# Performance work log

Hardware: AMD Instinct MI355X
Metric: run time of the kernel (lower is better)

Reference implementation:

```python
import jax, jax.numpy as jnp
import numpy as np

# Module constants (from source defaults)
KERNEL_SIZES = (2, 3, 4, 5)
KERNEL_NUMS = (2, 3, 4, 5)  # sum = 14 -> fc in_features
EMB_DIM = 100
NUM_CLASSES = 5
VOCAB = 100000
B, L = 512, 512


def setup_inputs() -> dict:
    key = jax.random.key(0)
    ks = jax.random.split(key, 12)
    words = jax.random.randint(ks[0], (B, L), 0, VOCAB)
    # Dense w2v table replacing the per-token vocab/gensim lookup (OOV rows would be zeros;
    # a random dense table is equivalent math for the gather).
    emb_table = jax.random.normal(ks[1], (VOCAB, EMB_DIM), dtype=jnp.float32) * 0.1
    inp = {"words": words, "emb_table": emb_table}
    for i, (ksz, knum) in enumerate(zip(KERNEL_SIZES, KERNEL_NUMS)):
        inp[f"w{ksz}"] = jax.random.normal(ks[2 + i], (knum, EMB_DIM, ksz), dtype=jnp.float32) * 0.05
        inp[f"b{ksz}"] = jnp.zeros((knum,), dtype=jnp.float32)
    inp["fc_w"] = jax.random.normal(ks[10], (NUM_CLASSES, sum(KERNEL_NUMS)), dtype=jnp.float32) * 0.1
    inp["fc_b"] = jnp.zeros((NUM_CLASSES,), dtype=jnp.float32)
    return inp


def _conv_relu_maxpool(x, w, b):
    # x: [B, D, L], w: [O, D, k] -> conv1d VALID, relu, max over time -> [B, O]
    y = jax.lax.conv_general_dilated(
        x, w, window_strides=(1,), padding="VALID",
        dimension_numbers=("NCH", "OIH", "NCH"))
    y = jax.nn.relu(y + b[None, :, None])
    return jnp.max(y, axis=-1)


def reference(words, emb_table, w2, b2, w3, b3, w4, b4, w5, b5, fc_w, fc_b):
    # Embedding gather (replaces the serial per-token Python loop)
    x = emb_table[words]                 # [B, L, D]
    x = jnp.transpose(x, (0, 2, 1))      # [B, D, L]
    feats = jnp.concatenate([
        _conv_relu_maxpool(x, w2, b2),
        _conv_relu_maxpool(x, w3, b3),
        _conv_relu_maxpool(x, w4, b4),
        _conv_relu_maxpool(x, w5, b5),
    ], axis=1)                           # [B, 14]
    # dropout is identity at inference
    return feats @ fc_w.T + fc_b         # [B, NUM_CLASSES]
```

## Files before the change

kernel.cpp:

```cpp
#include <hip/hip_runtime.h>
#include <hip/hip_bf16.h>

#define BATCH 512
#define SEQL  512
#define NCH   14
#define NCLS  5
#define DPAD  128
#define KSTEPS 20
#define POSB  64
#define ROWS  68
#define BLKS_PER_ROW 8
#define NBLK  (BATCH * BLKS_PER_ROW)
#define WS_B_BYTES 20480
#define BIAS_OFF   20480
#define FEAT_OFF   20544
#define NIT   9

typedef __attribute__((ext_vector_type(8))) short bf16x8;
typedef __attribute__((ext_vector_type(4))) float f32x4;

static __device__ __forceinline__ unsigned short bf16bits(float f) {
    __hip_bfloat16 h = __float2bfloat16(f);
    return __builtin_bit_cast(unsigned short, h);
}

__global__ void repack_w(
    const float* __restrict__ w2, const float* __restrict__ b2,
    const float* __restrict__ w3, const float* __restrict__ b3,
    const float* __restrict__ w4, const float* __restrict__ b4,
    const float* __restrict__ w5, const float* __restrict__ b5,
    unsigned short* __restrict__ wsb, float* __restrict__ biasf)
{
    const float* WP[4] = {w2, w3, w4, w5};
    const int gi = blockIdx.x * 256 + threadIdx.x;
    if (gi < WS_B_BYTES / 2) {
        int kstep = gi >> 9;
        int rem   = gi & 511;
        int l     = rem >> 3;
        int e     = rem & 7;
        int k     = kstep * 32 + ((l >> 4) << 3) + e;
        int n     = l & 15;
        int j     = k >> 7;
        int d     = k & 127;
        float v = 0.f;
        if (n < NCH && d < 100) {
            int kc = 2 + (n >= 2) + (n >= 5) + (n >= 9);
            if (j < kc) {
                int grp = (n >= 2) + (n >= 5) + (n >= 9);
                int ob  = (grp == 0) ? 0 : (grp == 1) ? 2 : (grp == 2) ? 5 : 9;
                v = WP[grp][((n - ob) * 100 + d) * kc + j];
            }
        }
        wsb[gi] = bf16bits(v);
    }
    if (blockIdx.x == 0 && threadIdx.x < 16) {
        const int t = threadIdx.x;
        float bv = 0.f;
        if (t < 2)        bv = b2[t];
        else if (t < 5)   bv = b3[t - 2];
        else if (t < 9)   bv = b4[t - 5];
        else if (t < NCH) bv = b5[t - 9];
        biasf[t] = bv;
    }
}

__global__ __launch_bounds__(256, 8) void cnn_mfma(
    const int* __restrict__ words,
    const float* __restrict__ emb,
    const char* __restrict__ ws,
    float* __restrict__ feats)
{
    __shared__ unsigned short xs[ROWS * DPAD];
    __shared__ float red[4][16];

    const int bid = blockIdx.x;
    const int b   = bid >> 3;
    const int blk = bid & 7;
    const int p0  = blk * POSB;
    const int tid = threadIdx.x;
    const int l   = tid & 63;
    const int wv  = tid >> 6;

    int toks[NIT];
    #pragma unroll
    for (int it = 0; it < NIT; ++it) {
        const int i = tid + it * 256;
        const int r = i >> 5;
        const int t = p0 + r;
        toks[it] = (i < ROWS * 32 && t < SEQL) ? words[b * SEQL + t] : -1;
    }

    const float4* __restrict__ emb4 = reinterpret_cast<const float4*>(emb);
    uint2* xs2 = reinterpret_cast<uint2*>(xs);
    #pragma unroll
    for (int it = 0; it < NIT; ++it) {
        const int i = tid + it * 256;
        if (i < ROWS * 32) {
            const int r = i >> 5;
            const int q = i & 31;
            uint lo = 0, hi = 0;
            if (toks[it] >= 0 && q < 25) {
                float4 x = emb4[(long)toks[it] * 25 + q];
                lo = (uint)bf16bits(x.x) | ((uint)bf16bits(x.y) << 16);
                hi = (uint)bf16bits(x.z) | ((uint)bf16bits(x.w) << 16);
            }
            const int addr = (r * 256 + q * 8) ^ ((r & 7) << 4);
            xs2[addr >> 3] = make_uint2(lo, hi);
        }
    }
    __syncthreads();

    f32x4 acc = {0.f, 0.f, 0.f, 0.f};
    const int m0 = wv * 16 + (l & 15);
    const int dl = (l >> 4) << 3;
    const char* xsb = reinterpret_cast<const char*>(xs);
    #pragma unroll
    for (int ks = 0; ks < KSTEPS; ++ks) {
        const int j  = ks >> 2;
        const int d0 = ((ks & 3) << 5) + dl;
        const int row = m0 + j;
        const int aad = (row * 256 + d0 * 2) ^ ((row & 7) << 4);
        bf16x8 a = *reinterpret_cast<const bf16x8*>(xsb + aad);
        bf16x8 bf = *reinterpret_cast<const bf16x8*>(ws + (ks * 64 + l) * 16);
        acc = __builtin_amdgcn_mfma_f32_16x16x32_bf16(a, bf, acc, 0, 0, 0);
    }

    const int ch  = l & 15;
    const int kch = 2 + (ch >= 2) + (ch >= 5) + (ch >= 9);
    const float bias = *reinterpret_cast<const float*>(ws + BIAS_OFF + ch * 4);
    const int rbase = (l >> 4) << 2;
    float v = 0.f;
    #pragma unroll
    for (int r = 0; r < 4; ++r) {
        const int t = p0 + wv * 16 + rbase + r;
        if (t + kch <= SEQL) v = fmaxf(v, fmaxf(acc[r] + bias, 0.f));
    }
    v = fmaxf(v, __shfl_xor(v, 16, 64));
    v = fmaxf(v, __shfl_xor(v, 32, 64));
    if (l < 16) red[wv][ch] = v;
    __syncthreads();

    if (tid < 16) {
        float f = fmaxf(fmaxf(red[0][tid], red[1][tid]),
                        fmaxf(red[2][tid], red[3][tid]));
        feats[bid * 16 + tid] = f;
    }
}

__global__ void fc_kernel(const float* __restrict__ feats,
                          const float* __restrict__ fcw,
                          const float* __restrict__ fcb,
                          float* __restrict__ out)
{
    const int i = blockIdx.x * 256 + threadIdx.x;
    if (i >= BATCH * NCLS) return;
    const int b   = i / NCLS;
    const int cls = i - b * NCLS;
    const float* fb = feats + b * (16 * BLKS_PER_ROW);
    float acc = fcb[cls];
    #pragma unroll
    for (int o = 0; o < NCH; ++o) {
        float f = fb[o];
        #pragma unroll
        for (int w = 1; w < BLKS_PER_ROW; ++w) f = fmaxf(f, fb[w * 16 + o]);
        acc += fcw[cls * NCH + o] * f;
    }
    out[i] = acc;
}

extern "C" void kernel_launch(void* const* d_in, const int* in_sizes, int n_in,
                              void* d_out, int out_size, void* d_ws, size_t ws_size,
                              hipStream_t stream) {
    const int*   words = (const int*)  d_in[0];
    const float* emb   = (const float*)d_in[1];
    const float* w2    = (const float*)d_in[2];
    const float* b2    = (const float*)d_in[3];
    const float* w3    = (const float*)d_in[4];
    const float* b3    = (const float*)d_in[5];
    const float* w4    = (const float*)d_in[6];
    const float* b4    = (const float*)d_in[7];
    const float* w5    = (const float*)d_in[8];
    const float* b5    = (const float*)d_in[9];
    const float* fcw   = (const float*)d_in[10];
    const float* fcb   = (const float*)d_in[11];
    float* out = (float*)d_out;
    char*  ws  = (char*)d_ws;

    unsigned short* wsb  = (unsigned short*)ws;
    float* biasf = (float*)(ws + BIAS_OFF);
    float* feats = (float*)(ws + FEAT_OFF);

    hipLaunchKernelGGL(repack_w, dim3(40), dim3(256), 0, stream,
                       w2, b2, w3, b3, w4, b4, w5, b5, wsb, biasf);
    hipLaunchKernelGGL(cnn_mfma, dim3(NBLK), dim3(256), 0, stream,
                       words, emb, ws, feats);
    hipLaunchKernelGGL(fc_kernel, dim3((BATCH * NCLS + 255) / 256), dim3(256), 0, stream,
                       feats, fcw, fcb, out);
}
```

Before: 39.71 us.

## Precompute per-vocab conv tap contributions then gather, max-pool and FC per batch

Instead of gathering embeddings per token and running the conv GEMM per position, a GEMM over the whole vocabulary table computes each word's contribution to every (tap, channel) pair and stores it as bf16. A second kernel gathers five contribution rows per position, sums the taps, applies bias, ReLU and max-pool, and folds in the FC layer, which removes the separate fc kernel. This trades work proportional to B*L*D for work proportional to VOCAB*D (a 40MB table read) and adds a 12.8MB intermediate write plus an extra bf16 rounding of the partial sums.

```diff
diff --git a/kernel.cpp b/kernel.cpp
--- a/kernel.cpp
+++ b/kernel.cpp
@@ -3,18 +3,14 @@
 
 #define BATCH 512
 #define SEQL  512
+#define VOCAB 100000
 #define NCH   14
 #define NCLS  5
-#define DPAD  128
-#define KSTEPS 20
-#define POSB  64
-#define ROWS  68
-#define BLKS_PER_ROW 8
-#define NBLK  (BATCH * BLKS_PER_ROW)
-#define WS_B_BYTES 20480
-#define BIAS_OFF   20480
-#define FEAT_OFF   20544
-#define NIT   9
+
+
+#define WSB_OFF     0
+#define BIAS_OFF    16384
+#define CONTRIB_OFF 32768
 
 typedef __attribute__((ext_vector_type(8))) short bf16x8;
 typedef __attribute__((ext_vector_type(4))) float f32x4;
@@ -22,6 +18,12 @@
 static __device__ __forceinline__ unsigned short bf16bits(float f) {
     __hip_bfloat16 h = __float2bfloat16(f);
     return __builtin_bit_cast(unsigned short, h);
+}
+static __device__ __forceinline__ float bf16f(unsigned int hbits) {
+    union { unsigned int u; float f; } x; x.u = hbits << 16; return x.f;
+}
+static __device__ __forceinline__ unsigned int getdw(const uint4& u, int w) {
+    switch (w) { case 0: return u.x; case 1: return u.y; case 2: return u.z; default: return u.w; }
 }
 
 __global__ void repack_w(
@@ -33,23 +35,25 @@
 {
     const float* WP[4] = {w2, w3, w4, w5};
     const int gi = blockIdx.x * 256 + threadIdx.x;
-    if (gi < WS_B_BYTES / 2) {
-        int kstep = gi >> 9;
-        int rem   = gi & 511;
-        int l     = rem >> 3;
-        int e     = rem & 7;
-        int k     = kstep * 32 + ((l >> 4) << 3) + e;
-        int n     = l & 15;
-        int j     = k >> 7;
-        int d     = k & 127;
+    if (gi < 8192) {
+        int nt = gi >> 11;
+        int ks = (gi >> 9) & 3;
+        int l  = (gi >> 3) & 63;
+        int e  = gi & 7;
+        int n  = nt * 16 + (l & 15);
+        int k  = ks * 32 + ((l >> 4) << 3) + e;
+        int j = -1, c = 0;
+        if (n < 14)                 { j = 0; c = n; }
+        else if (n >= 16 && n < 30) { j = 1; c = n - 16; }
+        else if (n >= 32 && n < 44) { j = 2; c = 2 + (n - 32); }
+        else if (n >= 44 && n < 53) { j = 3; c = 5 + (n - 44); }
+        else if (n >= 53 && n < 58) { j = 4; c = 9 + (n - 53); }
         float v = 0.f;
-        if (n < NCH && d < 100) {
-            int kc = 2 + (n >= 2) + (n >= 5) + (n >= 9);
-            if (j < kc) {
-                int grp = (n >= 2) + (n >= 5) + (n >= 9);
-                int ob  = (grp == 0) ? 0 : (grp == 1) ? 2 : (grp == 2) ? 5 : 9;
-                v = WP[grp][((n - ob) * 100 + d) * kc + j];
-            }
+        if (j >= 0 && k < 100) {
+            int kc  = 2 + (c >= 2) + (c >= 5) + (c >= 9);
+            int grp = (c >= 2) + (c >= 5) + (c >= 9);
+            int ob  = (grp == 0) ? 0 : (grp == 1) ? 2 : (grp == 2) ? 5 : 9;
+            v = WP[grp][((c - ob) * 100 + k) * kc + j];
         }
         wsb[gi] = bf16bits(v);
     }
@@ -64,108 +68,141 @@
     }
 }
 
-__global__ __launch_bounds__(256, 8) void cnn_mfma(
-    const int* __restrict__ words,
+__global__ __launch_bounds__(256, 4) void contrib_gemm(
     const float* __restrict__ emb,
     const char* __restrict__ ws,
-    float* __restrict__ feats)
+    unsigned short* __restrict__ contrib)
 {
-    __shared__ unsigned short xs[ROWS * DPAD];
-    __shared__ float red[4][16];
-
-    const int bid = blockIdx.x;
-    const int b   = bid >> 3;
-    const int blk = bid & 7;
-    const int p0  = blk * POSB;
+    __shared__ unsigned short xs[64 * 128];
+    const int v0  = blockIdx.x * 64;
     const int tid = threadIdx.x;
     const int l   = tid & 63;
-    const int wv  = tid >> 6;
-
-    int toks[NIT];
-    #pragma unroll
-    for (int it = 0; it < NIT; ++it) {
+    const int wt  = tid >> 6;
+
+    const float4* __restrict__ emb4 = reinterpret_cast<const float4*>(emb);
+    uint2* xs2 = reinterpret_cast<uint2*>(xs);
+    #pragma unroll
+    for (int it = 0; it < 8; ++it) {
         const int i = tid + it * 256;
         const int r = i >> 5;
-        const int t = p0 + r;
-        toks[it] = (i < ROWS * 32 && t < SEQL) ? words[b * SEQL + t] : -1;
-    }
-
-    const float4* __restrict__ emb4 = reinterpret_cast<const float4*>(emb);
-    uint2* xs2 = reinterpret_cast<uint2*>(xs);
-    #pragma unroll
-    for (int it = 0; it < NIT; ++it) {
-        const int i = tid + it * 256;
-        if (i < ROWS * 32) {
-            const int r = i >> 5;
-            const int q = i & 31;
-            uint lo = 0, hi = 0;
-            if (toks[it] >= 0 && q < 25) {
-                float4 x = emb4[(long)toks[it] * 25 + q];
-                lo = (uint)bf16bits(x.x) | ((uint)bf16bits(x.y) << 16);
-                hi = (uint)bf16bits(x.z) | ((uint)bf16bits(x.w) << 16);
+        const int q = i & 31;
+        const int v = v0 + r;
+        uint lo = 0, hi = 0;
+        if (v < VOCAB && q < 25) {
+            float4 x = emb4[(long)v * 25 + q];
+            lo = (uint)bf16bits(x.x) | ((uint)bf16bits(x.y) << 16);
+            hi = (uint)bf16bits(x.z) | ((uint)bf16bits(x.w) << 16);
+        }
+        const int addr = (r * 256 + q * 8) ^ ((r & 7) << 4);
+        xs2[addr >> 3] = make_uint2(lo, hi);
+    }
+    __syncthreads();
+
+    f32x4 acc[4] = {{0.f,0.f,0.f,0.f},{0.f,0.f,0.f,0.f},
+                    {0.f,0.f,0.f,0.f},{0.f,0.f,0.f,0.f}};
+    const char* xsb = reinterpret_cast<const char*>(xs);
+    const int arow = wt * 16 + (l & 15);
+    const int dl   = (l >> 4) << 3;
+    #pragma unroll
+    for (int ks = 0; ks < 4; ++ks) {
+        const int aad = (arow * 256 + (ks * 32 + dl) * 2) ^ ((arow & 7) << 4);
+        bf16x8 a = *reinterpret_cast<const bf16x8*>(xsb + aad);
+        #pragma unroll
+        for (int nt = 0; nt < 4; ++nt) {
+            bf16x8 bf = *reinterpret_cast<const bf16x8*>(
+                ws + WSB_OFF + ((nt * 4 + ks) * 64 + l) * 16);
+            acc[nt] = __builtin_amdgcn_mfma_f32_16x16x32_bf16(a, bf, acc[nt], 0, 0, 0);
+        }
+    }
+
+    const int vbase = v0 + wt * 16 + ((l >> 4) << 2);
+    #pragma unroll
+    for (int nt = 0; nt < 4; ++nt) {
+        #pragma unroll
+        for (int r = 0; r < 4; ++r) {
+            const int v = vbase + r;
+            if (v < VOCAB)
+                contrib[(long)v * 64 + nt * 16 + (l & 15)] = bf16bits(acc[nt][r]);
+        }
+    }
+}
+
+__global__ __launch_bounds__(512, 4) void gather_max_fc(
+    const int* __restrict__ words,
+    const unsigned short* __restrict__ contrib,
+    const float* __restrict__ biasf,
+    const float* __restrict__ fcw, const float* __restrict__ fcb,
+    float* __restrict__ out)
+{
+    __shared__ float red[8][NCH];
+    __shared__ float sfin[NCH];
+
+    const int b  = blockIdx.x;
+    const int t  = threadIdx.x;
+    const int l  = t & 63;
+    const int wv = t >> 6;
+
+    constexpr int KC[NCH]  = {2,2, 3,3,3, 4,4,4,4, 5,5,5,5,5};
+    constexpr int SIDX[5]  = {0,16,32,44,53};
+    constexpr int CST[5]   = {0,0,2,5,9};
+    constexpr int B0[5]    = {0,2,4,5,6};
+
+    int tok[5];
+    #pragma unroll
+    for (int j = 0; j < 5; ++j) {
+        int u = t + j; if (u > SEQL - 1) u = SEQL - 1;
+        tok[j] = words[b * SEQL + u];
+    }
+
+    uint4 u0[5], u1[5];
+    #pragma unroll
+    for (int j = 0; j < 5; ++j) {
+        const uint4* rp = reinterpret_cast<const uint4*>(contrib + (long)tok[j] * 64);
+        u0[j] = rp[B0[j]];
+        u1[j] = rp[B0[j] + 1];
+    }
+
+    float y[NCH];
+    #pragma unroll
+    for (int c = 0; c < NCH; ++c) {
+        float s = 0.f;
+        #pragma unroll
+        for (int j = 0; j < 5; ++j) {
+            if (j < KC[c]) {
+                const int n   = SIDX[j] + (c - CST[j]);
+                const int rel = 2 * n - 16 * B0[j];
+                const int w   = rel >> 2;
+                const int h   = (rel >> 1) & 1;
+                const unsigned int dw = (w < 4) ? getdw(u0[j], w) : getdw(u1[j], w - 4);
+                s += bf16f(h ? (dw >> 16) : (dw & 0xffffu));
             }
-            const int addr = (r * 256 + q * 8) ^ ((r & 7) << 4);
-            xs2[addr >> 3] = make_uint2(lo, hi);
-        }
+        }
+        y[c] = s;
+    }
+
+    #pragma unroll
+    for (int c = 0; c < NCH; ++c) {
+        float v = 0.f;
+        if (t + KC[c] <= SEQL) v = fmaxf(y[c] + biasf[c], 0.f);
+        #pragma unroll
+        for (int off = 32; off > 0; off >>= 1)
+            v = fmaxf(v, __shfl_xor(v, off, 64));
+        if (l == 0) red[wv][c] = v;
     }
     __syncthreads();
-
-    f32x4 acc = {0.f, 0.f, 0.f, 0.f};
-    const int m0 = wv * 16 + (l & 15);
-    const int dl = (l >> 4) << 3;
-    const char* xsb = reinterpret_cast<const char*>(xs);
-    #pragma unroll
-    for (int ks = 0; ks < KSTEPS; ++ks) {
-        const int j  = ks >> 2;
-        const int d0 = ((ks & 3) << 5) + dl;
-        const int row = m0 + j;
-        const int aad = (row * 256 + d0 * 2) ^ ((row & 7) << 4);
-        bf16x8 a = *reinterpret_cast<const bf16x8*>(xsb + aad);
-        bf16x8 bf = *reinterpret_cast<const bf16x8*>(ws + (ks * 64 + l) * 16);
-        acc = __builtin_amdgcn_mfma_f32_16x16x32_bf16(a, bf, acc, 0, 0, 0);
-    }
-
-    const int ch  = l & 15;
-    const int kch = 2 + (ch >= 2) + (ch >= 5) + (ch >= 9);
-    const float bias = *reinterpret_cast<const float*>(ws + BIAS_OFF + ch * 4);
-    const int rbase = (l >> 4) << 2;
-    float v = 0.f;
-    #pragma unroll
-    for (int r = 0; r < 4; ++r) {
-        const int t = p0 + wv * 16 + rbase + r;
-        if (t + kch <= SEQL) v = fmaxf(v, fmaxf(acc[r] + bias, 0.f));
-    }
-    v = fmaxf(v, __shfl_xor(v, 16, 64));
-    v = fmaxf(v, __shfl_xor(v, 32, 64));
-    if (l < 16) red[wv][ch] = v;
+    if (t < NCH) {
+        float f = red[0][t];
+        #pragma unroll
+        for (int w = 1; w < 8; ++w) f = fmaxf(f, red[w][t]);
+        sfin[t] = f;
+    }
     __syncthreads();
-
-    if (tid < 16) {
-        float f = fmaxf(fmaxf(red[0][tid], red[1][tid]),
-                        fmaxf(red[2][tid], red[3][tid]));
-        feats[bid * 16 + tid] = f;
-    }
-}
-
-__global__ void fc_kernel(const float* __restrict__ feats,
-                          const float* __restrict__ fcw,
-                          const float* __restrict__ fcb,
-                          float* __restrict__ out)
-{
-    const int i = blockIdx.x * 256 + threadIdx.x;
-    if (i >= BATCH * NCLS) return;
-    const int b   = i / NCLS;
-    const int cls = i - b * NCLS;
-    const float* fb = feats + b * (16 * BLKS_PER_ROW);
-    float acc = fcb[cls];
-    #pragma unroll
-    for (int o = 0; o < NCH; ++o) {
-        float f = fb[o];
-        #pragma unroll
-        for (int w = 1; w < BLKS_PER_ROW; ++w) f = fmaxf(f, fb[w * 16 + o]);
-        acc += fcw[cls * NCH + o] * f;
-    }
-    out[i] = acc;
+    if (t < NCLS) {
+        float acc = fcb[t];
+        #pragma unroll
+        for (int o = 0; o < NCH; ++o) acc += fcw[t * NCH + o] * sfin[o];
+        out[b * NCLS + t] = acc;
+    }
 }
 
 extern "C" void kernel_launch(void* const* d_in, const int* in_sizes, int n_in,
@@ -186,14 +223,14 @@
     float* out = (float*)d_out;
     char*  ws  = (char*)d_ws;
 
-    unsigned short* wsb  = (unsigned short*)ws;
-    float* biasf = (float*)(ws + BIAS_OFF);
-    float* feats = (float*)(ws + FEAT_OFF);
-
-    hipLaunchKernelGGL(repack_w, dim3(40), dim3(256), 0, stream,
+    unsigned short* wsb     = (unsigned short*)(ws + WSB_OFF);
+    float*          biasf   = (float*)(ws + BIAS_OFF);
+    unsigned short* contrib = (unsigned short*)(ws + CONTRIB_OFF);
+
+    hipLaunchKernelGGL(repack_w, dim3(32), dim3(256), 0, stream,
                        w2, b2, w3, b3, w4, b4, w5, b5, wsb, biasf);
-    hipLaunchKernelGGL(cnn_mfma, dim3(NBLK), dim3(256), 0, stream,
-                       words, emb, ws, feats);
-    hipLaunchKernelGGL(fc_kernel, dim3((BATCH * NCLS + 255) / 256), dim3(256), 0, stream,
-                       feats, fcw, fcb, out);
-}
+    hipLaunchKernelGGL(contrib_gemm, dim3((VOCAB + 63) / 64), dim3(256), 0, stream,
+                       emb, ws, contrib);
+    hipLaunchKernelGGL(gather_max_fc, dim3(BATCH), dim3(512), 0, stream,
+                       words, contrib, biasf, fcw, fcb, out);
+}
```

New measurement: 34.84 us (median of 3 runs). 12.3% less time.
